# Optimization experiments

Measured on AMD Instinct MI355X. Metric: run time of the kernel, lower is better.

## Reference

```python
import jax, jax.numpy as jnp
import numpy as np
import math

BS, SEQ, EMB, BD = 4, 2048, 512, 8
H = EMB // BD


def setup_inputs() -> dict:
    key = jax.random.key(0)
    ks = jax.random.split(key, 7)
    s = lambda fan: 1.0 / np.sqrt(fan)
    x = jax.random.normal(ks[0], (BS, SEQ, EMB), jnp.float32)
    # gen_block: Linear(EMB, EMB*BD) -> ReLU -> Linear(EMB*BD, EMB*BD)
    W1 = jax.random.normal(ks[1], (EMB * BD, EMB), jnp.float32) * s(EMB)
    b1 = jnp.zeros((EMB * BD,), jnp.float32)
    W2 = jax.random.normal(ks[2], (EMB * BD, EMB * BD), jnp.float32) * s(EMB * BD)
    b2 = jnp.zeros((EMB * BD,), jnp.float32)
    # gen_value: Linear(EMB, EMB) -> ReLU -> Linear(EMB, EMB)
    V1 = jax.random.normal(ks[3], (EMB, EMB), jnp.float32) * s(EMB)
    c1 = jnp.zeros((EMB,), jnp.float32)
    V2 = jax.random.normal(ks[4], (EMB, EMB), jnp.float32) * s(EMB)
    c2 = jnp.zeros((EMB,), jnp.float32)
    a0 = jax.random.normal(ks[5], (1, H, BD), jnp.float32)
    return {"x": x, "W1": W1, "b1": b1, "W2": W2, "b2": b2,
            "V1": V1, "c1": c1, "V2": V2, "c2": c2, "a0": a0}


def _forward(x, W1, b1, W2, b2, V1, c1, V2, c2, a0):
    bs, seq_len, emb = x.shape
    bd = BD
    h = emb // bd
    # block transition matrices: [bs, seq, h, bd, bd]
    blk = jax.nn.relu(x @ W1.T + b1) @ W2.T + b2
    blk = blk.reshape(bs, seq_len, h, bd, bd)
    blk = blk - blk.mean(axis=-2, keepdims=True)
    # p=1.2 norm over rows (dim=-2), then max over columns (dim=-1)
    norm = jnp.sum(jnp.abs(blk) ** 1.2, axis=-2, keepdims=True) ** (1.0 / 1.2)
    blk = blk / jnp.max(norm, axis=-1, keepdims=True)
    # values: [bs, seq, h, bd]
    v = (jax.nn.relu(x @ V1.T + c1) @ V2.T + c2).reshape(bs, seq_len, h, bd)

    log2_L = int(math.ceil(math.log2(seq_len + 1)))
    L = 2 ** log2_L
    n_zero = L - seq_len - 1
    # prepend a0 as initial state, pad to length L
    ev = jnp.concatenate([jnp.broadcast_to(a0, (bs, h, bd))[:, None], v], axis=1)
    a = jnp.pad(ev, ((0, 0), (0, n_zero), (0, 0), (0, 0)))  # [bs, L, h, bd]
    As = jnp.pad(blk, ((0, 0), (0, n_zero), (0, 0), (0, 0), (0, 0)))[:, :, None]  # [bs, L-1, 1, h, bd, bd]

    # Blelloch-style tree scan; log2_L levels, shapes shrink along n and grow along c
    for _ in range(log2_L):
        c = As.shape[2] * 2
        a = a.reshape(bs, L // c, c, h, bd)
        a1, a2 = a[:, :, :c // 2], a[:, :, c // 2:]
        coef = As[:, ::2]          # [bs, L//c, c//2, h, bd, bd]
        remain = As[:, 1::2]       # [bs, L//c - 1, c//2, h, bd, bd]
        prodd = jnp.einsum('bnchij,bnhjk->bnchik', coef[:, 1:], remain[:, :, -1])
        remain = jnp.concatenate([remain, prodd], axis=2)
        a2 = a2 + jnp.einsum('bnchij,bnhj->bnchi', coef, a1[:, :, -1])
        a = jnp.concatenate([a1, a2], axis=2)
        As = remain

    return a.reshape(bs, L, emb)[:, 1:seq_len + 1]


def reference(x, W1, b1, W2, b2, V1, c1, V2, c2, a0):
    return _forward(x, W1, b1, W2, b2, V1, c1, V2, c2, a0)
```

## Files before the change

### kernel.cpp

```cpp
#include <hip/hip_runtime.h>
#include <hip/hip_bf16.h>
#include <cstddef>


typedef _Float16 f16;
typedef _Float16 f16x4 __attribute__((ext_vector_type(4)));
typedef _Float16 f16x8 __attribute__((ext_vector_type(8)));
typedef float f32x4 __attribute__((ext_vector_type(4)));

__global__ __launch_bounds__(256)
void split_kernel(const float* __restrict__ in, f16* __restrict__ hi,
                  f16* __restrict__ lo, int n) {
  const int idx = (blockIdx.x * 256 + threadIdx.x) * 4;
  if (idx >= n) return;
  float4 v = *(const float4*)(in + idx);
  f16x4 h, l;
  h.x = (f16)v.x; l.x = (f16)(v.x - (float)h.x);
  h.y = (f16)v.y; l.y = (f16)(v.y - (float)h.y);
  h.z = (f16)v.z; l.z = (f16)(v.z - (float)h.z);
  h.w = (f16)v.w; l.w = (f16)(v.w - (float)h.w);
  *(f16x4*)(hi + idx) = h;
  *(f16x4*)(lo + idx) = l;
}

template<int EPI>
__global__ __launch_bounds__(256, 2)
void gemm_dma2(const f16* __restrict__ Ahi, const f16* __restrict__ Alo,
               const f16* __restrict__ Bhi, const f16* __restrict__ Blo,
               const float* __restrict__ bias, void* __restrict__ Ov,
               int M, int N, int K, int roff, int lg_mb) {
  __shared__ f16 S[2][4][128 * 32];
  const int tid = threadIdx.x, lane = tid & 63, wid = tid >> 6;
  const int total = gridDim.x, chunk = total >> 3;
  const int swz = (blockIdx.x & 7) * chunk + (blockIdx.x >> 3);
  const int mtile = swz & ((1 << lg_mb) - 1);
  const int ntile = swz >> lg_mb;
  const int m0 = mtile << 7, n0 = ntile << 7;
  const int wr = wid >> 1, wc = wid & 1;
  const int fr = lane & 15, g = lane >> 4;
  const int r_sub = lane >> 2, lc = lane & 3;

  f32x4 acc[4][4];
#pragma unroll
  for (int m = 0; m < 4; ++m)
#pragma unroll
    for (int n = 0; n < 4; ++n) acc[m][n] = (f32x4)0.f;

  const f16* gsrc = (wid == 0) ? Ahi + (size_t)m0 * K
                  : (wid == 1) ? Alo + (size_t)m0 * K
                  : (wid == 2) ? Bhi + (size_t)n0 * K
                               : Blo + (size_t)n0 * K;

  auto stage = [&](int b, int k0) {
    f16* ld = &S[b][wid][0];
#pragma unroll
    for (int i = 0; i < 8; ++i) {
      const int r = i * 16 + r_sub;
      const int sg = (lc - r - (r >> 2)) & 3;
      const f16* sp = gsrc + (size_t)r * K + k0 + sg * 8;
      __builtin_amdgcn_global_load_lds(
          (const __attribute__((address_space(1))) unsigned int*)sp,
          (__attribute__((address_space(3))) unsigned int*)(ld + i * 512),
          16, 0, 0);
    }
  };

  const int NT = K >> 5;
  stage(0, 0);
  __syncthreads();
  int cur = 0;
  for (int t = 0; t < NT; ++t) {
    if (t + 1 < NT) stage(cur ^ 1, (t + 1) << 5);
    f16x8 ah[4], al[4], bh[4], bl[4];
#pragma unroll
    for (int m = 0; m < 4; ++m) {
      const int rr = wr * 64 + m * 16 + fr;
      const int off = rr * 32 + (((g + rr + (rr >> 2)) & 3) << 3);
      ah[m] = *(const f16x8*)&S[cur][0][off];
      al[m] = *(const f16x8*)&S[cur][1][off];
    }
#pragma unroll
    for (int n = 0; n < 4; ++n) {
      const int rr = wc * 64 + n * 16 + fr;
      const int off = rr * 32 + (((g + rr + (rr >> 2)) & 3) << 3);
      bh[n] = *(const f16x8*)&S[cur][2][off];
      bl[n] = *(const f16x8*)&S[cur][3][off];
    }
#pragma unroll
    for (int m = 0; m < 4; ++m)
#pragma unroll
      for (int n = 0; n < 4; ++n) {
        acc[m][n] = __builtin_amdgcn_mfma_f32_16x16x32_f16(ah[m], bh[n], acc[m][n], 0, 0, 0);
        acc[m][n] = __builtin_amdgcn_mfma_f32_16x16x32_f16(ah[m], bl[n], acc[m][n], 0, 0, 0);
        acc[m][n] = __builtin_amdgcn_mfma_f32_16x16x32_f16(al[m], bh[n], acc[m][n], 0, 0, 0);
      }
    __syncthreads();
    cur ^= 1;
  }

  const int fq = lane >> 4;
  float bz[4];
#pragma unroll
  for (int n = 0; n < 4; ++n) bz[n] = bias[n0 + wc * 64 + n * 16 + fr];

  if (EPI == 0) {
    f16* Ohi = (f16*)Ov;
    f16* Olo = Ohi + (size_t)M * N;
#pragma unroll
    for (int m = 0; m < 4; ++m)
#pragma unroll
      for (int n = 0; n < 4; ++n) {
        const int col = n0 + wc * 64 + n * 16 + fr;
#pragma unroll
        for (int r = 0; r < 4; ++r) {
          const int row = m0 + wr * 64 + m * 16 + fq * 4 + r;
          float v = fmaxf(acc[m][n][r] + bz[n], 0.f);
          f16 h = (f16)v;
          f16 l = (f16)(v - (float)h);
          Ohi[(size_t)row * N + col] = h;
          Olo[(size_t)row * N + col] = l;
        }
      }
  } else if (EPI == 1) {
    float* O = (float*)Ov;
#pragma unroll
    for (int m = 0; m < 4; ++m) {
#pragma unroll
      for (int r = 0; r < 4; ++r) {
        float v[4];
#pragma unroll
        for (int n = 0; n < 4; ++n) v[n] = acc[m][n][r] + bz[n];
        float s = v[0] + v[1] + v[2] + v[3];
        s += __shfl_xor(s, 8);
        const float mean = s * 0.125f;
        float t = 0.f;
#pragma unroll
        for (int n = 0; n < 4; ++n) {
          v[n] -= mean;
          t += exp2f(1.2f * log2f(fabsf(v[n])));
        }
        t += __shfl_xor(t, 8);
        float nrm = exp2f((1.0f / 1.2f) * log2f(t));
        nrm = fmaxf(nrm, __shfl_xor(nrm, 1));
        nrm = fmaxf(nrm, __shfl_xor(nrm, 2));
        nrm = fmaxf(nrm, __shfl_xor(nrm, 4));
        const float inv = 1.f / nrm;
        const int row = m0 + wr * 64 + m * 16 + fq * 4 + r;
        const int grow = roff + row;
        const int bb = grow >> 11, ss = grow & 2047;
#pragma unroll
        for (int n = 0; n < 4; ++n) {
          const int col = n0 + wc * 64 + n * 16 + fr;
          O[(((size_t)(bb * 64 + (col >> 6)) * 2048 + ss) << 6) + (col & 63)] = v[n] * inv;
        }
      }
    }
  } else {
    float* O = (float*)Ov;
#pragma unroll
    for (int m = 0; m < 4; ++m)
#pragma unroll
      for (int n = 0; n < 4; ++n) {
        const int col = n0 + wc * 64 + n * 16 + fr;
#pragma unroll
        for (int r = 0; r < 4; ++r) {
          const int row = m0 + wr * 64 + m * 16 + fq * 4 + r;
          const int grow = roff + row;
          const int bb = grow >> 11, ss = grow & 2047;
          O[(((size_t)(bb * 64 + (col >> 3)) * 2048 + ss) << 3) + (col & 7)] = acc[m][n][r] + bz[n];
        }
      }
  }
}

#define SCH2 16
#define SEGL 128
#define NSEG 16

__global__ __launch_bounds__(256)
void scan_part1(const float* __restrict__ BLKT, const float* __restrict__ VT,
                float* __restrict__ Msum, float* __restrict__ Csum) {
  __shared__ __align__(16) float Abuf[4][2][SCH2 * 64];
  __shared__ __align__(16) float vbuf[4][2][SCH2 * 8];
  const int w = threadIdx.x >> 6, lane = threadIdx.x & 63;
  const int id = blockIdx.x * 4 + w;
  const int stream = id >> 4, t = id & 15;
  const int i = lane >> 3, j = lane & 7;
  const float* Ab = BLKT + (size_t)stream * (2048 * 64) + (size_t)t * (SEGL * 64);
  const float* Vb = VT + (size_t)stream * (2048 * 8) + (size_t)t * (SEGL * 8);

  float m = (i == j) ? 1.f : 0.f;
  float cj = 0.f;

  float4 ra[4]; float2 rv;
  auto loadc = [&](int c) {
    const float* sA = Ab + c * (SCH2 * 64);
#pragma unroll
    for (int q = 0; q < 4; ++q) ra[q] = *(const float4*)(sA + q * 256 + lane * 4);
    rv = *(const float2*)(Vb + c * (SCH2 * 8) + lane * 2);
  };
  auto store_lds = [&](int slot) {
#pragma unroll
    for (int q = 0; q < 4; ++q)
      *(float4*)&Abuf[w][slot][q * 256 + lane * 4] = ra[q];
    *(float2*)&vbuf[w][slot][lane * 2] = rv;
  };

  loadc(0); store_lds(0);
  int cur = 0;
  const int NC = SEGL / SCH2;
  for (int c = 0; c < NC; ++c) {
    if (c + 1 < NC) loadc(c + 1);
#pragma unroll
    for (int s = 0; s < SCH2; ++s) {
      const float aij = Abuf[w][cur][s * 64 + lane];
      float p = aij * cj;
      p += __shfl_xor(p, 1);
      p += __shfl_xor(p, 2);
      p += __shfl_xor(p, 4);
      const float cn = p + vbuf[w][cur][s * 8 + i];
      cj = __shfl(cn, j << 3);
      float arow[8];
      *(float4*)&arow[0] = *(const float4*)&Abuf[w][cur][s * 64 + i * 8];
      *(float4*)&arow[4] = *(const float4*)&Abuf[w][cur][s * 64 + i * 8 + 4];
      float mn = 0.f;
#pragma unroll
      for (int k = 0; k < 8; ++k)
        mn = fmaf(arow[k], __shfl(m, (k << 3) | j), mn);
      m = mn;
    }
    if (c + 1 < NC) store_lds(cur ^ 1);
    cur ^= 1;
  }
  Msum[(size_t)id * 64 + lane] = m;
  if (lane < 8) Csum[(size_t)id * 8 + lane] = cj;
}

__global__ __launch_bounds__(64)
void scan_part2(const float* __restrict__ Msum, const float* __restrict__ Csum,
                const float* __restrict__ a0, float* __restrict__ Ybnd) {
  const int stream = blockIdx.x;
  const int lane = threadIdx.x;
  const int i = lane >> 3, j = lane & 7;
  const int h = stream & 63;
  float y = a0[h * 8 + j];
  for (int t = 0; t < NSEG; ++t) {
    const size_t sid = (size_t)stream * NSEG + t;
    if (lane < 8) Ybnd[sid * 8 + lane] = y;
    float p = Msum[sid * 64 + lane] * y;
    p += __shfl_xor(p, 1);
    p += __shfl_xor(p, 2);
    p += __shfl_xor(p, 4);
    const float yn = p + Csum[sid * 8 + i];
    y = __shfl(yn, j << 3);
  }
}

__global__ __launch_bounds__(256)
void scan_part3(const float* __restrict__ BLKT, const float* __restrict__ VT,
                const float* __restrict__ Ybnd, float* __restrict__ out) {
  __shared__ __align__(16) float Abuf[4][2][SCH2 * 64];
  __shared__ __align__(16) float vbuf[4][2][SCH2 * 8];
  const int w = threadIdx.x >> 6, lane = threadIdx.x & 63;
  const int id = blockIdx.x * 4 + w;
  const int stream = id >> 4, t = id & 15;
  const int b = stream >> 6, h = stream & 63;
  const int i = lane >> 3, j = lane & 7;
  const float* Ab = BLKT + (size_t)stream * (2048 * 64) + (size_t)t * (SEGL * 64);
  const float* Vb = VT + (size_t)stream * (2048 * 8) + (size_t)t * (SEGL * 8);
  float* ob = out + (size_t)b * (2048 * 512) + (size_t)(t * SEGL) * 512 + h * 8;

  float y = Ybnd[(size_t)id * 8 + j];

  float4 ra[4]; float2 rv;
  auto loadc = [&](int c) {
    const float* sA = Ab + c * (SCH2 * 64);
#pragma unroll
    for (int q = 0; q < 4; ++q) ra[q] = *(const float4*)(sA + q * 256 + lane * 4);
    rv = *(const float2*)(Vb + c * (SCH2 * 8) + lane * 2);
  };
  auto store_lds = [&](int slot) {
#pragma unroll
    for (int q = 0; q < 4; ++q)
      *(float4*)&Abuf[w][slot][q * 256 + lane * 4] = ra[q];
    *(float2*)&vbuf[w][slot][lane * 2] = rv;
  };

  loadc(0); store_lds(0);
  int cur = 0;
  const int NC = SEGL / SCH2;
  for (int c = 0; c < NC; ++c) {
    if (c + 1 < NC) loadc(c + 1);
#pragma unroll
    for (int s = 0; s < SCH2; ++s) {
      const float aij = Abuf[w][cur][s * 64 + lane];
      float p = aij * y;
      p += __shfl_xor(p, 1);
      p += __shfl_xor(p, 2);
      p += __shfl_xor(p, 4);
      const float yn = p + vbuf[w][cur][s * 8 + i];
      if (j == 0) ob[(size_t)(c * SCH2 + s) * 512 + i] = yn;
      y = __shfl(yn, j << 3);
    }
    if (c + 1 < NC) store_lds(cur ^ 1);
    cur ^= 1;
  }
}

extern "C" void kernel_launch(void* const* d_in, const int* in_sizes, int n_in,
                              void* d_out, int out_size, void* d_ws, size_t ws_size,
                              hipStream_t stream) {
  const float* x  = (const float*)d_in[0];
  const float* W1 = (const float*)d_in[1];
  const float* b1 = (const float*)d_in[2];
  const float* W2 = (const float*)d_in[3];
  const float* b2 = (const float*)d_in[4];
  const float* V1 = (const float*)d_in[5];
  const float* c1 = (const float*)d_in[6];
  const float* V2 = (const float*)d_in[7];
  const float* c2 = (const float*)d_in[8];
  const float* a0 = (const float*)d_in[9];
  float* out = (float*)d_out;

  dim3 blk(256);

  char* base = (char*)d_ws;
  float* BLKT = (float*)base;
  float* VT   = (float*)(base + 134217728ull);
  f16* W2hi   = (f16*)(base + 150994944ull);
  f16* W2lo   = (f16*)(base + 184549376ull);
  f16* H1hi   = (f16*)(base + 218103808ull);
  f16* xchi   = (f16*)(base + 251658240ull);
  f16* xclo   = (f16*)(base + 253755392ull);
  f16* W1hi   = (f16*)(base + 255852544ull);
  f16* W1lo   = (f16*)(base + 260046848ull);
  f16* V1hi   = (f16*)(base + 264241152ull);
  f16* V1lo   = (f16*)(base + 264765440ull);
  f16* V2hi   = (f16*)(base + 265289728ull);
  f16* V2lo   = (f16*)(base + 265814016ull);
  float* Msum = (float*)(base + 266338304ull);
  float* Csum = (float*)(base + 267386880ull);
  float* Ybnd = (float*)(base + 267517952ull);
  f16* xfhi   = W2hi;
  f16* xflo   = W2hi + 4194304ull;
  f16* HVhi   = H1hi;

  split_kernel<<<4096, blk, 0, stream>>>(x, xfhi, xflo, 4194304);
  split_kernel<<<256, blk, 0, stream>>>(V1, V1hi, V1lo, 262144);
  split_kernel<<<256, blk, 0, stream>>>(V2, V2hi, V2lo, 262144);
  gemm_dma2<0><<<256, blk, 0, stream>>>(
      xfhi, xflo, V1hi, V1lo, c1, HVhi, 8192, 512, 512, 0, 6);
  gemm_dma2<2><<<256, blk, 0, stream>>>(
      HVhi, HVhi + (size_t)8192 * 512, V2hi, V2lo, c2, VT, 8192, 512, 512, 0, 6);

  split_kernel<<<2048, blk, 0, stream>>>(W1, W1hi, W1lo, 2097152);
  split_kernel<<<16384, blk, 0, stream>>>(W2, W2hi, W2lo, 16777216);

  for (int c = 0; c < 4; ++c) {
    const float* xc = x + (size_t)c * 2048 * 512;
    split_kernel<<<1024, blk, 0, stream>>>(xc, xchi, xclo, 1048576);
    gemm_dma2<0><<<512, blk, 0, stream>>>(
        xchi, xclo, W1hi, W1lo, b1, H1hi, 2048, 4096, 512, 0, 4);
    gemm_dma2<1><<<512, blk, 0, stream>>>(
        H1hi, H1hi + (size_t)2048 * 4096, W2hi, W2lo, b2, BLKT,
        2048, 4096, 4096, c * 2048, 4);
  }
  scan_part1<<<1024, blk, 0, stream>>>(BLKT, VT, Msum, Csum);
  scan_part2<<<256, 64, 0, stream>>>(Msum, Csum, a0, Ybnd);
  scan_part3<<<1024, blk, 0, stream>>>(BLKT, VT, Ybnd, out);
}
```

Baseline: 1.099 ms.

## Use 256x256 tile GEMM with 512 threads and chunk scan per two batches

Adds a gemm_big kernel with 256x256 output tiles and 8 waves per block for the large W1/W2 GEMMs, raising operand reuse per LDS load. The x split is now done once up front instead of per chunk. Work is processed in two chunks of 4096 rows, and the three scan kernels run per chunk so the BLKT buffer shrinks to half size and stays more cache-friendly. Risks include higher register pressure from the 8x4 accumulator array, which could limit occupancy, and a grid of only 256 blocks per GEMM.

```diff
diff --git a/kernel.cpp b/kernel.cpp
--- a/kernel.cpp
+++ b/kernel.cpp
@@ -21,6 +21,138 @@
   h.w = (f16)v.w; l.w = (f16)(v.w - (float)h.w);
   *(f16x4*)(hi + idx) = h;
   *(f16x4*)(lo + idx) = l;
+}
+
+template<int EPI>
+__global__ __launch_bounds__(512, 2)
+void gemm_big(const f16* __restrict__ Ahi, const f16* __restrict__ Alo,
+              const f16* __restrict__ Bhi, const f16* __restrict__ Blo,
+              const float* __restrict__ bias, void* __restrict__ Ov,
+              int M, int N, int K, int roff) {
+  __shared__ f16 S[2][4][256 * 32];
+  const int tid = threadIdx.x, lane = tid & 63, wid = tid >> 6;
+  const int m0 = blockIdx.y << 8, n0 = blockIdx.x << 8;
+  const int wr = wid >> 2, wc = wid & 3;
+  const int fr = lane & 15, g = lane >> 4;
+  const int r_sub = lane >> 2, lc = lane & 3;
+  const int p = wid >> 1, half = wid & 1;
+
+  f32x4 acc[8][4];
+#pragma unroll
+  for (int m = 0; m < 8; ++m)
+#pragma unroll
+    for (int n = 0; n < 4; ++n) acc[m][n] = (f32x4)0.f;
+
+  const f16* gsrc = (p == 0) ? Ahi + (size_t)m0 * K
+                  : (p == 1) ? Alo + (size_t)m0 * K
+                  : (p == 2) ? Bhi + (size_t)n0 * K
+                             : Blo + (size_t)n0 * K;
+
+  auto stage = [&](int b, int k0) {
+    f16* ld = &S[b][p][half * 4096];
+#pragma unroll
+    for (int i = 0; i < 8; ++i) {
+      const int r = half * 128 + i * 16 + r_sub;
+      const int sg = (lc - r - (r >> 2)) & 3;
+      const f16* sp = gsrc + (size_t)r * K + k0 + sg * 8;
+      __builtin_amdgcn_global_load_lds(
+          (const __attribute__((address_space(1))) unsigned int*)sp,
+          (__attribute__((address_space(3))) unsigned int*)(ld + i * 512),
+          16, 0, 0);
+    }
+  };
+
+  const int NT = K >> 5;
+  stage(0, 0);
+  __syncthreads();
+  int cur = 0;
+  for (int t = 0; t < NT; ++t) {
+    if (t + 1 < NT) stage(cur ^ 1, (t + 1) << 5);
+    f16x8 ah[8], al[8], bh[4], bl[4];
+#pragma unroll
+    for (int m = 0; m < 8; ++m) {
+      const int rr = wr * 128 + m * 16 + fr;
+      const int off = rr * 32 + (((g + rr + (rr >> 2)) & 3) << 3);
+      ah[m] = *(const f16x8*)&S[cur][0][off];
+      al[m] = *(const f16x8*)&S[cur][1][off];
+    }
+#pragma unroll
+    for (int n = 0; n < 4; ++n) {
+      const int rr = wc * 64 + n * 16 + fr;
+      const int off = rr * 32 + (((g + rr + (rr >> 2)) & 3) << 3);
+      bh[n] = *(const f16x8*)&S[cur][2][off];
+      bl[n] = *(const f16x8*)&S[cur][3][off];
+    }
+#pragma unroll
+    for (int m = 0; m < 8; ++m)
+#pragma unroll
+      for (int n = 0; n < 4; ++n) {
+        acc[m][n] = __builtin_amdgcn_mfma_f32_16x16x32_f16(ah[m], bh[n], acc[m][n], 0, 0, 0);
+        acc[m][n] = __builtin_amdgcn_mfma_f32_16x16x32_f16(ah[m], bl[n], acc[m][n], 0, 0, 0);
+        acc[m][n] = __builtin_amdgcn_mfma_f32_16x16x32_f16(al[m], bh[n], acc[m][n], 0, 0, 0);
+      }
+    __syncthreads();
+    cur ^= 1;
+  }
+
+  const int fq = lane >> 4;
+  float bz[4];
+#pragma unroll
+  for (int n = 0; n < 4; ++n) bz[n] = bias[n0 + wc * 64 + n * 16 + fr];
+
+  if (EPI == 0) {
+    f16* Ohi = (f16*)Ov;
+    f16* Olo = Ohi + (size_t)M * N;
+#pragma unroll
+    for (int m = 0; m < 8; ++m)
+#pragma unroll
+      for (int n = 0; n < 4; ++n) {
+        const int col = n0 + wc * 64 + n * 16 + fr;
+#pragma unroll
+        for (int r = 0; r < 4; ++r) {
+          const int row = m0 + wr * 128 + m * 16 + fq * 4 + r;
+          float v = fmaxf(acc[m][n][r] + bz[n], 0.f);
+          f16 h = (f16)v;
+          f16 l = (f16)(v - (float)h);
+          Ohi[(size_t)row * N + col] = h;
+          Olo[(size_t)row * N + col] = l;
+        }
+      }
+  } else {
+    float* O = (float*)Ov;
+#pragma unroll
+    for (int m = 0; m < 8; ++m) {
+#pragma unroll
+      for (int r = 0; r < 4; ++r) {
+        float v[4];
+#pragma unroll
+        for (int n = 0; n < 4; ++n) v[n] = acc[m][n][r] + bz[n];
+        float s = v[0] + v[1] + v[2] + v[3];
+        s += __shfl_xor(s, 8);
+        const float mean = s * 0.125f;
+        float t = 0.f;
+#pragma unroll
+        for (int n = 0; n < 4; ++n) {
+          v[n] -= mean;
+          t += exp2f(1.2f * log2f(fabsf(v[n])));
+        }
+        t += __shfl_xor(t, 8);
+        float nrm = exp2f((1.0f / 1.2f) * log2f(t));
+        nrm = fmaxf(nrm, __shfl_xor(nrm, 1));
+        nrm = fmaxf(nrm, __shfl_xor(nrm, 2));
+        nrm = fmaxf(nrm, __shfl_xor(nrm, 4));
+        const float inv = 1.f / nrm;
+        const int row = m0 + wr * 128 + m * 16 + fq * 4 + r;
+        const int grow = roff + row;
+        const int bb = grow >> 11, ss = grow & 2047;
+#pragma unroll
+        for (int n = 0; n < 4; ++n) {
+          const int col = n0 + wc * 64 + n * 16 + fr;
+          O[(((size_t)(bb * 64 + (col >> 6)) * 2048 + ss) << 6) + (col & 63)] = v[n] * inv;
+        }
+      }
+    }
+  }
 }
 
 template<int EPI>
@@ -121,40 +253,6 @@
           Olo[(size_t)row * N + col] = l;
         }
       }
-  } else if (EPI == 1) {
-    float* O = (float*)Ov;
-#pragma unroll
-    for (int m = 0; m < 4; ++m) {
-#pragma unroll
-      for (int r = 0; r < 4; ++r) {
-        float v[4];
-#pragma unroll
-        for (int n = 0; n < 4; ++n) v[n] = acc[m][n][r] + bz[n];
-        float s = v[0] + v[1] + v[2] + v[3];
-        s += __shfl_xor(s, 8);
-        const float mean = s * 0.125f;
-        float t = 0.f;
-#pragma unroll
-        for (int n = 0; n < 4; ++n) {
-          v[n] -= mean;
-          t += exp2f(1.2f * log2f(fabsf(v[n])));
-        }
-        t += __shfl_xor(t, 8);
-        float nrm = exp2f((1.0f / 1.2f) * log2f(t));
-        nrm = fmaxf(nrm, __shfl_xor(nrm, 1));
-        nrm = fmaxf(nrm, __shfl_xor(nrm, 2));
-        nrm = fmaxf(nrm, __shfl_xor(nrm, 4));
-        const float inv = 1.f / nrm;
-        const int row = m0 + wr * 64 + m * 16 + fq * 4 + r;
-        const int grow = roff + row;
-        const int bb = grow >> 11, ss = grow & 2047;
-#pragma unroll
-        for (int n = 0; n < 4; ++n) {
-          const int col = n0 + wc * 64 + n * 16 + fr;
-          O[(((size_t)(bb * 64 + (col >> 6)) * 2048 + ss) << 6) + (col & 63)] = v[n] * inv;
-        }
-      }
-    }
   } else {
     float* O = (float*)Ov;
 #pragma unroll
@@ -178,7 +276,7 @@
 #define NSEG 16
 
 __global__ __launch_bounds__(256)
-void scan_part1(const float* __restrict__ BLKT, const float* __restrict__ VT,
+void scan_part1(const float* __restrict__ BLKTc, const float* __restrict__ VTc,
                 float* __restrict__ Msum, float* __restrict__ Csum) {
   __shared__ __align__(16) float Abuf[4][2][SCH2 * 64];
   __shared__ __align__(16) float vbuf[4][2][SCH2 * 8];
@@ -186,8 +284,8 @@
   const int id = blockIdx.x * 4 + w;
   const int stream = id >> 4, t = id & 15;
   const int i = lane >> 3, j = lane & 7;
-  const float* Ab = BLKT + (size_t)stream * (2048 * 64) + (size_t)t * (SEGL * 64);
-  const float* Vb = VT + (size_t)stream * (2048 * 8) + (size_t)t * (SEGL * 8);
+  const float* Ab = BLKTc + (size_t)stream * (2048 * 64) + (size_t)t * (SEGL * 64);
+  const float* Vb = VTc + (size_t)stream * (2048 * 8) + (size_t)t * (SEGL * 8);
 
   float m = (i == j) ? 1.f : 0.f;
   float cj = 0.f;
@@ -257,8 +355,8 @@
 }
 
 __global__ __launch_bounds__(256)
-void scan_part3(const float* __restrict__ BLKT, const float* __restrict__ VT,
-                const float* __restrict__ Ybnd, float* __restrict__ out) {
+void scan_part3(const float* __restrict__ BLKTc, const float* __restrict__ VTc,
+                const float* __restrict__ Ybnd, float* __restrict__ outc) {
   __shared__ __align__(16) float Abuf[4][2][SCH2 * 64];
   __shared__ __align__(16) float vbuf[4][2][SCH2 * 8];
   const int w = threadIdx.x >> 6, lane = threadIdx.x & 63;
@@ -266,9 +364,9 @@
   const int stream = id >> 4, t = id & 15;
   const int b = stream >> 6, h = stream & 63;
   const int i = lane >> 3, j = lane & 7;
-  const float* Ab = BLKT + (size_t)stream * (2048 * 64) + (size_t)t * (SEGL * 64);
-  const float* Vb = VT + (size_t)stream * (2048 * 8) + (size_t)t * (SEGL * 8);
-  float* ob = out + (size_t)b * (2048 * 512) + (size_t)(t * SEGL) * 512 + h * 8;
+  const float* Ab = BLKTc + (size_t)stream * (2048 * 64) + (size_t)t * (SEGL * 64);
+  const float* Vb = VTc + (size_t)stream * (2048 * 8) + (size_t)t * (SEGL * 8);
+  float* ob = outc + (size_t)b * (2048 * 512) + (size_t)(t * SEGL) * 512 + h * 8;
 
   float y = Ybnd[(size_t)id * 8 + j];
 
@@ -325,47 +423,47 @@
   dim3 blk(256);
 
   char* base = (char*)d_ws;
-  float* BLKT = (float*)base;
-  float* VT   = (float*)(base + 134217728ull);
-  f16* W2hi   = (f16*)(base + 150994944ull);
-  f16* W2lo   = (f16*)(base + 184549376ull);
-  f16* H1hi   = (f16*)(base + 218103808ull);
-  f16* xchi   = (f16*)(base + 251658240ull);
-  f16* xclo   = (f16*)(base + 253755392ull);
-  f16* W1hi   = (f16*)(base + 255852544ull);
-  f16* W1lo   = (f16*)(base + 260046848ull);
-  f16* V1hi   = (f16*)(base + 264241152ull);
-  f16* V1lo   = (f16*)(base + 264765440ull);
-  f16* V2hi   = (f16*)(base + 265289728ull);
-  f16* V2lo   = (f16*)(base + 265814016ull);
-  float* Msum = (float*)(base + 266338304ull);
-  float* Csum = (float*)(base + 267386880ull);
-  float* Ybnd = (float*)(base + 267517952ull);
-  f16* xfhi   = W2hi;
-  f16* xflo   = W2hi + 4194304ull;
+  f16* W2hi   = (f16*)base;
+  f16* W2lo   = (f16*)(base + 33554432ull);
+  f16* H1hi   = (f16*)(base + 67108864ull);
+  float* BLKTc= (float*)(base + 134217728ull);
+  float* VT   = (float*)(base + 201326592ull);
+  f16* xfhi   = (f16*)(base + 218103808ull);
+  f16* xflo   = (f16*)(base + 226492416ull);
+  f16* W1hi   = (f16*)(base + 234881024ull);
+  f16* W1lo   = (f16*)(base + 239075328ull);
+  f16* V1hi   = (f16*)(base + 243269632ull);
+  f16* V1lo   = (f16*)(base + 243793920ull);
+  f16* V2hi   = (f16*)(base + 244318208ull);
+  f16* V2lo   = (f16*)(base + 244842496ull);
+  float* Msum = (float*)(base + 245366784ull);
+  float* Csum = (float*)(base + 245891072ull);
+  float* Ybnd = (float*)(base + 245956608ull);
   f16* HVhi   = H1hi;
 
   split_kernel<<<4096, blk, 0, stream>>>(x, xfhi, xflo, 4194304);
+  split_kernel<<<2048, blk, 0, stream>>>(W1, W1hi, W1lo, 2097152);
+  split_kernel<<<16384, blk, 0, stream>>>(W2, W2hi, W2lo, 16777216);
   split_kernel<<<256, blk, 0, stream>>>(V1, V1hi, V1lo, 262144);
   split_kernel<<<256, blk, 0, stream>>>(V2, V2hi, V2lo, 262144);
+
   gemm_dma2<0><<<256, blk, 0, stream>>>(
       xfhi, xflo, V1hi, V1lo, c1, HVhi, 8192, 512, 512, 0, 6);
   gemm_dma2<2><<<256, blk, 0, stream>>>(
       HVhi, HVhi + (size_t)8192 * 512, V2hi, V2lo, c2, VT, 8192, 512, 512, 0, 6);
 
-  split_kernel<<<2048, blk, 0, stream>>>(W1, W1hi, W1lo, 2097152);
-  split_kernel<<<16384, blk, 0, stream>>>(W2, W2hi, W2lo, 16777216);
-
-  for (int c = 0; c < 4; ++c) {
-    const float* xc = x + (size_t)c * 2048 * 512;
-    split_kernel<<<1024, blk, 0, stream>>>(xc, xchi, xclo, 1048576);
-    gemm_dma2<0><<<512, blk, 0, stream>>>(
-        xchi, xclo, W1hi, W1lo, b1, H1hi, 2048, 4096, 512, 0, 4);
-    gemm_dma2<1><<<512, blk, 0, stream>>>(
-        H1hi, H1hi + (size_t)2048 * 4096, W2hi, W2lo, b2, BLKT,
-        2048, 4096, 4096, c * 2048, 4);
-  }
-  scan_part1<<<1024, blk, 0, stream>>>(BLKT, VT, Msum, Csum);
-  scan_part2<<<256, 64, 0, stream>>>(Msum, Csum, a0, Ybnd);
-  scan_part3<<<1024, blk, 0, stream>>>(BLKT, VT, Ybnd, out);
-}
+  for (int c = 0; c < 2; ++c) {
+    const f16* xahi = xfhi + (size_t)c * 4096 * 512;
+    const f16* xalo = xflo + (size_t)c * 4096 * 512;
+    gemm_big<0><<<dim3(16, 16), 512, 0, stream>>>(
+        xahi, xalo, W1hi, W1lo, b1, H1hi, 4096, 4096, 512, 0);
+    gemm_big<1><<<dim3(16, 16), 512, 0, stream>>>(
+        H1hi, H1hi + (size_t)4096 * 4096, W2hi, W2lo, b2, BLKTc,
+        4096, 4096, 4096, 0);
+    const float* VTc = VT + (size_t)c * 2 * 64 * 2048 * 8;
+    float* outc = out + (size_t)c * 2 * 2048 * 512;
+    scan_part1<<<512, blk, 0, stream>>>(BLKTc, VTc, Msum, Csum);
+    scan_part2<<<128, 64, 0, stream>>>(Msum, Csum, a0, Ybnd);
+    scan_part3<<<512, blk, 0, stream>>>(BLKTc, VTc, Ybnd, outc);
+  }
+}
```

Result: faster. 954.3 us (-13.2%).
